# Performance work log

Measured on AMD Instinct MI355X. Metric: run time of the kernel, lower is better.

The kernel has to match this reference:

```python
import jax, jax.numpy as jnp
import numpy as np

ROPE_BASE = 10000.0

def _rope(x):
    # x: (B, T, H, hd); rotate-half RoPE
    B, T, H, hd = x.shape
    half = hd // 2
    inv_freq = 1.0 / (ROPE_BASE ** (jnp.arange(half, dtype=jnp.float32) / half))
    ang = jnp.arange(T, dtype=jnp.float32)[:, None] * inv_freq[None, :]  # (T, half)
    cos = jnp.cos(ang)[None, :, None, :]
    sin = jnp.sin(ang)[None, :, None, :]
    x1, x2 = x[..., :half], x[..., half:]
    return jnp.concatenate([x1 * cos - x2 * sin, x1 * sin + x2 * cos], axis=-1)

def setup_inputs() -> dict:
    key = jax.random.key(0)
    k1, k2, k3 = jax.random.split(key, 3)
    B, T, D = 4, 2048, 2048
    x = jax.random.normal(k1, (B, T, D), dtype=jnp.float32)
    attn_mask = jnp.ones((B, T), dtype=bool)
    w_qkv = jax.random.normal(k2, (3 * D, D), dtype=jnp.float32) * (D ** -0.5)
    w_out = jax.random.normal(k3, (D, D), dtype=jnp.float32) * (D ** -0.5)
    return {"x": x, "attn_mask": attn_mask, "is_causal": 1, "w_qkv": w_qkv, "w_out": w_out}

def reference(x, attn_mask, is_causal, w_qkv, w_out):
    B, T, D = x.shape
    H = 16
    hd = D // H
    qkv = jnp.einsum('btd,ed->bte', x, w_qkv)  # (B, T, 3D)
    q, k, v = jnp.split(qkv, 3, axis=2)
    q = _rope(q.reshape(B, T, H, hd))
    k = _rope(k.reshape(B, T, H, hd))
    v = v.reshape(B, T, H, hd)
    scale = 1.0 / jnp.sqrt(jnp.float32(hd))
    scores = jnp.einsum('bqhd,bkhd->bhqk', q, k) * scale  # (B, H, T, T)
    if is_causal:
        mask = jnp.tril(jnp.ones((T, T), dtype=bool))[None, None]
    else:
        mask = attn_mask[:, None, None, :]  # (B,1,1,T)
    scores = jnp.where(mask, scores, jnp.finfo(scores.dtype).min)
    attn = jax.nn.softmax(scores, axis=-1)
    y = jnp.einsum('bhqk,bkhd->bqhd', attn, v).reshape(B, T, D)
    return jnp.einsum('btd,ed->bte', y, w_out)
```

## Files before the change

kernel.cpp:

```cpp
#include <hip/hip_runtime.h>
#include <stdint.h>
#include <stddef.h>

typedef float f32x4 __attribute__((ext_vector_type(4)));
typedef __bf16 bf16x8 __attribute__((ext_vector_type(8)));
typedef short s16x4 __attribute__((ext_vector_type(4)));

#define DEVI static __device__ __forceinline__

DEVI float bf2f(unsigned short u) {
  unsigned int x = ((unsigned int)u) << 16;
  float f;
  __builtin_memcpy(&f, &x, 4);
  return f;
}
DEVI unsigned short f2bf(float f) {
  unsigned int x;
  __builtin_memcpy(&x, &f, 4);
  unsigned int r = (x + 0x7fffu + ((x >> 16) & 1u)) >> 16;
  return (unsigned short)r;
}

DEVI void async16(const void* g, void* l) {
  __builtin_amdgcn_global_load_lds((__attribute__((address_space(1))) void*)g,
                                   (__attribute__((address_space(3))) void*)l,
                                   16, 0, 0);
}

#define BAR_LGKM()                                          \
  do {                                                      \
    asm volatile("s_waitcnt lgkmcnt(0)" ::: "memory");      \
    __builtin_amdgcn_s_barrier();                           \
    __builtin_amdgcn_sched_barrier(0);                      \
  } while (0)

#define BAR_VM(N)                                               \
  do {                                                          \
    asm volatile("s_waitcnt vmcnt(" #N ")" ::: "memory");       \
    __builtin_amdgcn_s_barrier();                               \
    __builtin_amdgcn_sched_barrier(0);                          \
  } while (0)

__global__ __launch_bounds__(256) void cvt_bf16(const float* __restrict__ in,
                                                unsigned short* __restrict__ out, int n) {
  int i = (blockIdx.x * 256 + threadIdx.x) * 4;
  if (i >= n) return;
  float4 v = *(const float4*)(in + i);
  s16x4 o;
  o[0] = (short)f2bf(v.x);
  o[1] = (short)f2bf(v.y);
  o[2] = (short)f2bf(v.z);
  o[3] = (short)f2bf(v.w);
  *(s16x4*)(out + i) = o;
}

__global__ __launch_bounds__(256) void rope_table(float* __restrict__ tab) {
  int idx = blockIdx.x * 256 + threadIdx.x;
  if (idx >= 2048 * 64) return;
  int tt = idx >> 6, j = idx & 63;
  float inv = powf(10000.0f, -(float)j * (1.0f / 64.0f));
  float ang = (float)tt * inv;
  tab[tt * 128 + j] = cosf(ang);
  tab[tt * 128 + 64 + j] = sinf(ang);
}

__global__ __launch_bounds__(256) void rope_apply(unsigned short* __restrict__ Qg,
                                                  unsigned short* __restrict__ Kg,
                                                  const float* __restrict__ tab) {
  const float S2 = 0.0883883476483184f * 1.44269504088896341f;
  int idx = blockIdx.x * 256 + threadIdx.x;
  int j4 = idx & 15;
  int tt = (idx >> 4) & 2047;
  int bh = idx >> 15;
  size_t base = ((size_t)bh * 2048 + tt) * 128;
  f32x4 c4 = *(const f32x4*)(tab + tt * 128 + j4 * 4);
  f32x4 s4 = *(const f32x4*)(tab + tt * 128 + 64 + j4 * 4);
  s16x4 q1 = *(const s16x4*)(Qg + base + j4 * 4);
  s16x4 q2 = *(const s16x4*)(Qg + base + 64 + j4 * 4);
  s16x4 k1 = *(const s16x4*)(Kg + base + j4 * 4);
  s16x4 k2 = *(const s16x4*)(Kg + base + 64 + j4 * 4);
  s16x4 o1, o2, p1, p2;
#pragma unroll
  for (int r = 0; r < 4; ++r) {
    float c = c4[r], s = s4[r];
    float a = bf2f((unsigned short)q1[r]), b2 = bf2f((unsigned short)q2[r]);
    o1[r] = (short)f2bf((a * c - b2 * s) * S2);
    o2[r] = (short)f2bf((a * s + b2 * c) * S2);
    float ka = bf2f((unsigned short)k1[r]), kb = bf2f((unsigned short)k2[r]);
    p1[r] = (short)f2bf(ka * c - kb * s);
    p2[r] = (short)f2bf(ka * s + kb * c);
  }
  *(s16x4*)(Qg + base + j4 * 4) = o1;
  *(s16x4*)(Qg + base + 64 + j4 * 4) = o2;
  *(s16x4*)(Kg + base + j4 * 4) = p1;
  *(s16x4*)(Kg + base + 64 + j4 * 4) = p2;
}

template <int EPI>
__global__ __launch_bounds__(512) void gemm256(const unsigned short* __restrict__ A,
                                               const unsigned short* __restrict__ B,
                                               float* __restrict__ C, int M, int N, int K,
                                               unsigned short* __restrict__ Q,
                                               unsigned short* __restrict__ Kk,
                                               unsigned short* __restrict__ VT) {
  __shared__ __attribute__((aligned(128))) unsigned short Al[2][2][8192];
  __shared__ __attribute__((aligned(128))) unsigned short Bl[2][2][8192];
  const int t = threadIdx.x;
  const int lane = t & 63;
  const int w = t >> 6, wr = w >> 2, wc = w & 3;
  const int g = lane >> 4, lr = lane & 15;

  const int id = blockIdx.y * gridDim.x + blockIdx.x;
  const int mt = M >> 8, nt = N >> 8;
  const int xcd = id & 7;
  const int local = id >> 3;
  const int rm = mt >> 2, rn = nt >> 1;
  const int bm = ((xcd & 3) * rm + (local % rm)) * 256;
  const int bn = ((xcd >> 2) * rn + (local / rm)) * 256;

  const unsigned short* aptr = A + (size_t)bm * K;
  const unsigned short* bptr = B + (size_t)bn * K;

  const int srow = t >> 3;
  const int sslot = (t & 7) ^ (srow & 7);

#define STG(arr, mat, p, h, kt)                                                   \
  do {                                                                            \
    const unsigned short* _s =                                                    \
        (mat) + (size_t)((h) * 128 + srow) * K + (size_t)(kt) * 64 + sslot * 8;   \
    async16(_s, &arr[p][h][t * 8]);                                               \
    async16(_s + (size_t)64 * K, &arr[p][h][t * 8 + 4096]);                       \
  } while (0)

  const int u0 = ((g ^ (lr & 7)) * 8) + lr * 64;
  const int u1 = (((4 + g) ^ (lr & 7)) * 8) + lr * 64;

#define LDA_(p, mh)                                                               \
  _Pragma("unroll") for (int mf = 0; mf < 4; ++mf) {                              \
    af[mf][0] = *(const bf16x8*)&Al[p][wr][(mh) * 4096 + mf * 1024 + u0];         \
    af[mf][1] = *(const bf16x8*)&Al[p][wr][(mh) * 4096 + mf * 1024 + u1];         \
  }
#define LDB_(dst, p, nh)                                                          \
  _Pragma("unroll") for (int nf = 0; nf < 2; ++nf) {                              \
    dst[nf][0] = *(const bf16x8*)&Bl[p][wc >> 1][(wc & 1) * 4096 + (nh) * 2048 +  \
                                                 nf * 1024 + u0];                 \
    dst[nf][1] = *(const bf16x8*)&Bl[p][wc >> 1][(wc & 1) * 4096 + (nh) * 2048 +  \
                                                 nf * 1024 + u1];                 \
  }
#define MMA_(bsrc, mh, nh)                                                        \
  __builtin_amdgcn_s_setprio(1);                                                  \
  _Pragma("unroll") for (int mf = 0; mf < 4; ++mf)                                \
      _Pragma("unroll") for (int nf = 0; nf < 2; ++nf) {                          \
    acc[(mh) * 4 + mf][(nh) * 2 + nf] = __builtin_amdgcn_mfma_f32_16x16x32_bf16(  \
        af[mf][0], bsrc[nf][0], acc[(mh) * 4 + mf][(nh) * 2 + nf], 0, 0, 0);      \
    acc[(mh) * 4 + mf][(nh) * 2 + nf] = __builtin_amdgcn_mfma_f32_16x16x32_bf16(  \
        af[mf][1], bsrc[nf][1], acc[(mh) * 4 + mf][(nh) * 2 + nf], 0, 0, 0);      \
  }                                                                               \
  __builtin_amdgcn_s_setprio(0);
#define BARR() __builtin_amdgcn_s_barrier();

  f32x4 acc[8][4] = {};
  bf16x8 af[4][2], bfrA[2][2], bfrB[2][2];

  STG(Al, aptr, 0, 0, 0);
  STG(Al, aptr, 0, 1, 0);
  STG(Bl, bptr, 0, 0, 0);
  STG(Bl, bptr, 0, 1, 0);
  STG(Bl, bptr, 1, 0, 1);
  STG(Bl, bptr, 1, 1, 1);
  asm volatile("s_waitcnt vmcnt(4)" ::: "memory");
  __builtin_amdgcn_s_barrier();

  const int NITER = K >> 7;
  for (int i = 0; i < NITER; ++i) {
    const bool G = (i + 1 < NITER);
    const int t1 = 2 * i + 1, t2 = 2 * i + 2, t3 = 2 * i + 3;

    LDA_(0, 0);
    LDB_(bfrA, 0, 0);
    STG(Al, aptr, 1, 0, t1);
    STG(Al, aptr, 1, 1, t1);
    BARR();
    MMA_(bfrA, 0, 0);
    BARR();
    LDB_(bfrB, 0, 1);
    BARR();
    MMA_(bfrB, 0, 1);
    BARR();
    LDA_(0, 1);
    BARR();
    MMA_(bfrB, 1, 1);
    BARR();
    if (G) {
      STG(Bl, bptr, 0, 0, t2);
      asm volatile("s_waitcnt vmcnt(2)" ::: "memory");
    } else {
      asm volatile("s_waitcnt vmcnt(0)" ::: "memory");
    }
    BARR();
    MMA_(bfrA, 1, 0);
    BARR();
    LDA_(1, 0);
    LDB_(bfrA, 1, 0);
    if (G) STG(Bl, bptr, 0, 1, t2);
    BARR();
    MMA_(bfrA, 0, 0);
    BARR();
    LDB_(bfrB, 1, 1);
    if (G) STG(Al, aptr, 0, 0, t2);
    BARR();
    MMA_(bfrB, 0, 1);
    BARR();
    LDA_(1, 1);
    if (G) STG(Al, aptr, 0, 1, t2);
    BARR();
    MMA_(bfrB, 1, 1);
    BARR();
    if (G) {
      STG(Bl, bptr, 1, 0, t3);
      STG(Bl, bptr, 1, 1, t3);
      asm volatile("s_waitcnt vmcnt(4)" ::: "memory");
    }
    BARR();
    MMA_(bfrA, 1, 0);
    BARR();
  }
#undef STG
#undef LDA_
#undef LDB_
#undef MMA_
#undef BARR

  if (EPI == 0) {
#pragma unroll
    for (int mp = 0; mp < 8; ++mp) {
      int m0 = bm + wr * 128 + (mp >> 2) * 64 + (mp & 3) * 16 + g * 4;
#pragma unroll
      for (int nfi = 0; nfi < 4; ++nfi) {
        int n = bn + wc * 64 + (nfi >> 1) * 32 + (nfi & 1) * 16 + lr;
#pragma unroll
        for (int r = 0; r < 4; ++r) C[(size_t)(m0 + r) * N + n] = acc[mp][nfi][r];
      }
    }
  } else {
    const int bi = bm >> 11;
    const int tbase = bm & 2047;
#pragma unroll
    for (int nfi = 0; nfi < 4; ++nfi) {
      int e = bn + wc * 64 + (nfi >> 1) * 32 + (nfi & 1) * 16 + lr;
      int region = e >> 11;
      int e2 = e & 2047;
      int h = e2 >> 7, d = e2 & 127;
      int bh = bi * 16 + h;
#pragma unroll
      for (int mp = 0; mp < 8; ++mp) {
        int trow = tbase + wr * 128 + (mp >> 2) * 64 + (mp & 3) * 16 + g * 4;
        if (region == 2) {
          s16x4 pk;
#pragma unroll
          for (int r = 0; r < 4; ++r) pk[r] = (short)f2bf(acc[mp][nfi][r]);
          *(s16x4*)(VT + ((size_t)bh * 128 + d) * 2048 + trow) = pk;
        } else {
          unsigned short* dst = (region == 0) ? Q : Kk;
#pragma unroll
          for (int r = 0; r < 4; ++r)
            dst[((size_t)bh * 2048 + trow + r) * 128 + d] = f2bf(acc[mp][nfi][r]);
        }
      }
    }
  }
}

__global__ __launch_bounds__(256) void flash_attn(const unsigned short* __restrict__ Qg,
                                                  const unsigned short* __restrict__ Kg,
                                                  const unsigned short* __restrict__ VTg,
                                                  unsigned short* __restrict__ Yg,
                                                  const int* __restrict__ iscausal,
                                                  const unsigned char* __restrict__ amask) {
  __shared__ __attribute__((aligned(128))) unsigned short Ks[2][64 * 128];
  __shared__ __attribute__((aligned(128))) unsigned short Vs[2][128 * 64];
  __shared__ __attribute__((aligned(128))) unsigned short Ps[4][16 * 72];

  const int t = threadIdx.x, lane = t & 63, w = t >> 6;
  const int g = lane >> 4, lr = lane & 15;
  const int id = blockIdx.x;
  const int xcd = id & 7, j5 = id >> 3;
  const int bh = xcd * 8 + (j5 >> 5);
  const int qbi = 31 - (j5 & 31);
  const int b = bh >> 4;
  const int qb = qbi * 64;
  const int causal = iscausal[0] != 0;
  const int nt = causal ? (qbi + 1) : 32;

  const unsigned short* qrow = Qg + ((size_t)bh * 2048 + qb + w * 16 + lr) * 128;
  bf16x8 qf[4];
#pragma unroll
  for (int ds = 0; ds < 4; ++ds) qf[ds] = *(const bf16x8*)(qrow + ds * 32 + g * 8);

  const unsigned short* Kbase = Kg + (size_t)bh * 2048 * 128;
  const unsigned short* Vbase = VTg + (size_t)bh * 128 * 2048;

  const int rK = t >> 4, sK = ((t & 15) ^ rK);
  const int rV = t >> 3, sV = ((t & 7) ^ ((t >> 3) & 7));

#define STAGE(KT, P)                                                                    \
  do {                                                                                  \
    const int _kv = (KT) * 64;                                                          \
    _Pragma("unroll") for (int c = 0; c < 4; ++c)                                       \
        async16(Kbase + (size_t)(_kv + c * 16 + rK) * 128 + sK * 8,                     \
                &Ks[P][c * 2048 + t * 8]);                                              \
    _Pragma("unroll") for (int c = 0; c < 4; ++c)                                       \
        async16(Vbase + (size_t)(c * 32 + rV) * 2048 + _kv + sV * 8,                    \
                &Vs[P][c * 2048 + t * 8]);                                              \
  } while (0)

  unsigned int oi[4] = {0x3F803F80u, 0x3F803F80u, 0x3F803F80u, 0x3F803F80u};
  bf16x8 ones;
  __builtin_memcpy(&ones, oi, 16);

  f32x4 acc[8] = {};
  f32x4 accl = {0.f, 0.f, 0.f, 0.f};
  float mrow[4] = {-1e30f, -1e30f, -1e30f, -1e30f};

  STAGE(0, 0);

  for (int kt = 0; kt < nt; ++kt) {
    const int p = kt & 1;
    const int kv0 = kt * 64;
    if (kt + 1 < nt) {
      STAGE(kt + 1, p ^ 1);
      BAR_VM(8);
    } else {
      BAR_VM(0);
    }

    f32x4 s[4] = {};
    __builtin_amdgcn_s_setprio(1);
#pragma unroll
    for (int cf = 0; cf < 4; ++cf)
#pragma unroll
      for (int ds = 0; ds < 4; ++ds) {
        bf16x8 kf = *(const bf16x8*)(&Ks[p][(cf * 16 + lr) * 128 + (((ds * 4 + g) ^ lr) * 8)]);
        s[cf] = __builtin_amdgcn_mfma_f32_16x16x32_bf16(qf[ds], kf, s[cf], 0, 0, 0);
      }
    __builtin_amdgcn_s_setprio(0);

    const int q0 = qb + w * 16 + g * 4;
    if (causal) {
      if (kt == qbi) {
#pragma unroll
        for (int cf = 0; cf < 4; ++cf) {
          int kvg = kv0 + cf * 16 + lr;
#pragma unroll
          for (int r = 0; r < 4; ++r)
            if (kvg > q0 + r) s[cf][r] = -1e30f;
        }
      }
    } else {
#pragma unroll
      for (int cf = 0; cf < 4; ++cf) {
        int kvg = kv0 + cf * 16 + lr;
        if (!amask[(size_t)b * 2048 + kvg]) {
#pragma unroll
          for (int r = 0; r < 4; ++r) s[cf][r] = -1e30f;
        }
      }
    }

    f32x4 lm;
#pragma unroll
    for (int r = 0; r < 4; ++r)
      lm[r] = fmaxf(fmaxf(s[0][r], s[1][r]), fmaxf(s[2][r], s[3][r]));
    bool ok = true;
#pragma unroll
    for (int r = 0; r < 4; ++r) ok = ok && (lm[r] <= mrow[r] + 8.0f);
    if (!__all(ok)) {
      f32x4 mx = lm;
#pragma unroll
      for (int off = 8; off >= 1; off >>= 1)
#pragma unroll
        for (int r = 0; r < 4; ++r) mx[r] = fmaxf(mx[r], __shfl_xor(mx[r], off));
#pragma unroll
      for (int r = 0; r < 4; ++r) {
        float mn = fmaxf(mrow[r], mx[r]);
        float corr = exp2f(mrow[r] - mn);
        mrow[r] = mn;
        accl[r] *= corr;
#pragma unroll
        for (int jf = 0; jf < 8; ++jf) acc[jf][r] *= corr;
      }
    }

#pragma unroll
    for (int cf = 0; cf < 4; ++cf)
#pragma unroll
      for (int r = 0; r < 4; ++r) s[cf][r] = exp2f(s[cf][r] - mrow[r]);

    unsigned short* Pw = &Ps[w][0];
#pragma unroll
    for (int cf = 0; cf < 4; ++cf)
#pragma unroll
      for (int r = 0; r < 4; ++r) Pw[(g * 4 + r) * 72 + cf * 16 + lr] = f2bf(s[cf][r]);
    asm volatile("s_waitcnt lgkmcnt(0)" ::: "memory");
    __builtin_amdgcn_sched_barrier(0);

    bf16x8 pa0 = *(const bf16x8*)(Pw + lr * 72 + g * 8);
    bf16x8 pa1 = *(const bf16x8*)(Pw + lr * 72 + 32 + g * 8);

    accl = __builtin_amdgcn_mfma_f32_16x16x32_bf16(pa0, ones, accl, 0, 0, 0);
    accl = __builtin_amdgcn_mfma_f32_16x16x32_bf16(pa1, ones, accl, 0, 0, 0);

    __builtin_amdgcn_s_setprio(1);
#pragma unroll
    for (int jf = 0; jf < 8; ++jf) {
      bf16x8 v0 = *(const bf16x8*)(&Vs[p][(jf * 16 + lr) * 64 + ((g ^ (lr & 7)) * 8)]);
      bf16x8 v1 = *(const bf16x8*)(&Vs[p][(jf * 16 + lr) * 64 + (((4 + g) ^ (lr & 7)) * 8)]);
      acc[jf] = __builtin_amdgcn_mfma_f32_16x16x32_bf16(pa0, v0, acc[jf], 0, 0, 0);
      acc[jf] = __builtin_amdgcn_mfma_f32_16x16x32_bf16(pa1, v1, acc[jf], 0, 0, 0);
    }
    __builtin_amdgcn_s_setprio(0);

    BAR_LGKM();
  }
#undef STAGE

  const int h = bh & 15;
  float rl[4];
#pragma unroll
  for (int r = 0; r < 4; ++r) rl[r] = __builtin_amdgcn_rcpf(accl[r]);
#pragma unroll
  for (int jf = 0; jf < 8; ++jf)
#pragma unroll
    for (int r = 0; r < 4; ++r) {
      int tt = qb + w * 16 + g * 4 + r;
      Yg[((size_t)b * 2048 + tt) * 2048 + h * 128 + jf * 16 + lr] = f2bf(acc[jf][r] * rl[r]);
    }
}

extern "C" void kernel_launch(void* const* d_in, const int* in_sizes, int n_in, void* d_out,
                              int out_size, void* d_ws, size_t ws_size, hipStream_t stream) {
  const float* x = (const float*)d_in[0];
  const unsigned char* amask = (const unsigned char*)d_in[1];
  const int* iscausal = (const int*)d_in[2];
  const float* wqkv = (const float*)d_in[3];
  const float* wout = (const float*)d_in[4];
  float* out = (float*)d_out;

  const size_t MT = 8192, D = 2048, ND = 6144;
  unsigned short* xb = (unsigned short*)d_ws;
  unsigned short* wqkvb = xb + MT * D;
  unsigned short* woutb = wqkvb + ND * D;
  unsigned short* q = woutb + D * D;
  unsigned short* k = q + MT * D;
  unsigned short* vt = k + MT * D;
  unsigned short* y = vt + MT * D;
  float* tab = (float*)(y + MT * D);
  if (ws_size < (size_t)(100663296) * 2 + 2048 * 128 * 4) return;

  cvt_bf16<<<dim3(16384), dim3(256), 0, stream>>>(x, xb, (int)(MT * D));
  cvt_bf16<<<dim3(12288), dim3(256), 0, stream>>>(wqkv, wqkvb, (int)(ND * D));
  cvt_bf16<<<dim3(4096), dim3(256), 0, stream>>>(wout, woutb, (int)(D * D));
  rope_table<<<dim3(512), dim3(256), 0, stream>>>(tab);
  gemm256<1><<<dim3(24, 32), dim3(512), 0, stream>>>(xb, wqkvb, nullptr, 8192, 6144, 2048, q, k, vt);
  rope_apply<<<dim3(8192), dim3(256), 0, stream>>>(q, k, tab);
  flash_attn<<<dim3(2048), dim3(256), 0, stream>>>(q, k, vt, y, iscausal, amask);
  gemm256<0><<<dim3(8, 32), dim3(512), 0, stream>>>(y, woutb, out, 8192, 2048, 2048, nullptr,
                                                    nullptr, nullptr);
}
```

Baseline: 486.2 us.

## Enlarge flash-attention query tile to 128 rows with 8 waves and fuse bf16 conversions

Flash attention now runs 512-thread blocks, each covering 128 query rows with 8 waves, so every staged K/V tile is shared by twice as many waves. This halves the K/V global traffic per query. The block-to-tile mapping is reordered to pair long and short causal tiles for load balance, and the causal mask check becomes a per-wave condition. The three fp32-to-bf16 conversion launches are merged into a single kernel to cut launch overhead. In exchange, the larger blocks may lower occupancy and leave wider causal tail imbalance, and the rewritten mask and index logic carries some correctness risk.

```diff
diff --git a/kernel.cpp b/kernel.cpp
--- a/kernel.cpp
+++ b/kernel.cpp
@@ -26,6 +26,13 @@
                                    (__attribute__((address_space(3))) void*)l,
                                    16, 0, 0);
 }
+
+#define BAR_VM(N)                                               \
+  do {                                                          \
+    asm volatile("s_waitcnt vmcnt(" #N ")" ::: "memory");       \
+    __builtin_amdgcn_s_barrier();                               \
+    __builtin_amdgcn_sched_barrier(0);                          \
+  } while (0)
 
 #define BAR_LGKM()                                          \
   do {                                                      \
@@ -34,24 +41,31 @@
     __builtin_amdgcn_sched_barrier(0);                      \
   } while (0)
 
-#define BAR_VM(N)                                               \
-  do {                                                          \
-    asm volatile("s_waitcnt vmcnt(" #N ")" ::: "memory");       \
-    __builtin_amdgcn_s_barrier();                               \
-    __builtin_amdgcn_sched_barrier(0);                          \
-  } while (0)
-
-__global__ __launch_bounds__(256) void cvt_bf16(const float* __restrict__ in,
-                                                unsigned short* __restrict__ out, int n) {
+__global__ __launch_bounds__(256) void cvt3(const float* __restrict__ x,
+                                            const float* __restrict__ wq,
+                                            const float* __restrict__ wo,
+                                            unsigned short* __restrict__ xb,
+                                            unsigned short* __restrict__ wqb,
+                                            unsigned short* __restrict__ wob) {
+  const int n1 = 16777216, n2 = 12582912;
   int i = (blockIdx.x * 256 + threadIdx.x) * 4;
-  if (i >= n) return;
-  float4 v = *(const float4*)(in + i);
+  const float* src;
+  unsigned short* dst;
+  int off;
+  if (i < n1) {
+    src = x; dst = xb; off = i;
+  } else if (i < n1 + n2) {
+    src = wq; dst = wqb; off = i - n1;
+  } else {
+    src = wo; dst = wob; off = i - n1 - n2;
+  }
+  float4 v = *(const float4*)(src + off);
   s16x4 o;
   o[0] = (short)f2bf(v.x);
   o[1] = (short)f2bf(v.y);
   o[2] = (short)f2bf(v.z);
   o[3] = (short)f2bf(v.w);
-  *(s16x4*)(out + i) = o;
+  *(s16x4*)(dst + off) = o;
 }
 
 __global__ __launch_bounds__(256) void rope_table(float* __restrict__ tab) {
@@ -271,7 +285,7 @@
   }
 }
 
-__global__ __launch_bounds__(256) void flash_attn(const unsigned short* __restrict__ Qg,
+__global__ __launch_bounds__(512) void flash_attn(const unsigned short* __restrict__ Qg,
                                                   const unsigned short* __restrict__ Kg,
                                                   const unsigned short* __restrict__ VTg,
                                                   unsigned short* __restrict__ Yg,
@@ -279,18 +293,19 @@
                                                   const unsigned char* __restrict__ amask) {
   __shared__ __attribute__((aligned(128))) unsigned short Ks[2][64 * 128];
   __shared__ __attribute__((aligned(128))) unsigned short Vs[2][128 * 64];
-  __shared__ __attribute__((aligned(128))) unsigned short Ps[4][16 * 72];
+  __shared__ __attribute__((aligned(128))) unsigned short Ps[8][16 * 72];
 
   const int t = threadIdx.x, lane = t & 63, w = t >> 6;
   const int g = lane >> 4, lr = lane & 15;
   const int id = blockIdx.x;
   const int xcd = id & 7, j5 = id >> 3;
-  const int bh = xcd * 8 + (j5 >> 5);
-  const int qbi = 31 - (j5 & 31);
+  const int rr = j5 >> 3;
+  const int qbi = (rr < 4) ? (15 - rr) : (rr < 8) ? (rr - 4) : (rr < 12) ? (19 - rr) : (rr - 8);
+  const int bh = xcd * 8 + (j5 & 7);
   const int b = bh >> 4;
-  const int qb = qbi * 64;
+  const int qb = qbi * 128;
   const int causal = iscausal[0] != 0;
-  const int nt = causal ? (qbi + 1) : 32;
+  const int nt = causal ? (2 * qbi + 2) : 32;
 
   const unsigned short* qrow = Qg + ((size_t)bh * 2048 + qb + w * 16 + lr) * 128;
   bf16x8 qf[4];
@@ -300,18 +315,18 @@
   const unsigned short* Kbase = Kg + (size_t)bh * 2048 * 128;
   const unsigned short* Vbase = VTg + (size_t)bh * 128 * 2048;
 
-  const int rK = t >> 4, sK = ((t & 15) ^ rK);
-  const int rV = t >> 3, sV = ((t & 7) ^ ((t >> 3) & 7));
+  const int rK = t >> 4, sK = (t & 15) ^ (rK & 15);
+  const int rV = t >> 3, sV = (t & 7) ^ (rV & 7);
 
 #define STAGE(KT, P)                                                                    \
   do {                                                                                  \
     const int _kv = (KT) * 64;                                                          \
-    _Pragma("unroll") for (int c = 0; c < 4; ++c)                                       \
-        async16(Kbase + (size_t)(_kv + c * 16 + rK) * 128 + sK * 8,                     \
-                &Ks[P][c * 2048 + t * 8]);                                              \
-    _Pragma("unroll") for (int c = 0; c < 4; ++c)                                       \
-        async16(Vbase + (size_t)(c * 32 + rV) * 2048 + _kv + sV * 8,                    \
-                &Vs[P][c * 2048 + t * 8]);                                              \
+    _Pragma("unroll") for (int c = 0; c < 2; ++c)                                       \
+        async16(Kbase + (size_t)(_kv + c * 32 + rK) * 128 + sK * 8,                     \
+                &Ks[P][c * 4096 + t * 8]);                                              \
+    _Pragma("unroll") for (int c = 0; c < 2; ++c)                                       \
+        async16(Vbase + (size_t)(c * 64 + rV) * 2048 + _kv + sV * 8,                    \
+                &Vs[P][c * 4096 + t * 8]);                                              \
   } while (0)
 
   unsigned int oi[4] = {0x3F803F80u, 0x3F803F80u, 0x3F803F80u, 0x3F803F80u};
@@ -329,7 +344,7 @@
     const int kv0 = kt * 64;
     if (kt + 1 < nt) {
       STAGE(kt + 1, p ^ 1);
-      BAR_VM(8);
+      BAR_VM(4);
     } else {
       BAR_VM(0);
     }
@@ -345,9 +360,10 @@
       }
     __builtin_amdgcn_s_setprio(0);
 
-    const int q0 = qb + w * 16 + g * 4;
+    const int qw = qb + w * 16;
+    const int q0 = qw + g * 4;
     if (causal) {
-      if (kt == qbi) {
+      if (kv0 + 63 > qw) {
 #pragma unroll
         for (int cf = 0; cf < 4; ++cf) {
           int kvg = kv0 + cf * 16 + lr;
@@ -457,13 +473,11 @@
   float* tab = (float*)(y + MT * D);
   if (ws_size < (size_t)(100663296) * 2 + 2048 * 128 * 4) return;
 
-  cvt_bf16<<<dim3(16384), dim3(256), 0, stream>>>(x, xb, (int)(MT * D));
-  cvt_bf16<<<dim3(12288), dim3(256), 0, stream>>>(wqkv, wqkvb, (int)(ND * D));
-  cvt_bf16<<<dim3(4096), dim3(256), 0, stream>>>(wout, woutb, (int)(D * D));
+  cvt3<<<dim3(32768), dim3(256), 0, stream>>>(x, wqkv, wout, xb, wqkvb, woutb);
   rope_table<<<dim3(512), dim3(256), 0, stream>>>(tab);
   gemm256<1><<<dim3(24, 32), dim3(512), 0, stream>>>(xb, wqkvb, nullptr, 8192, 6144, 2048, q, k, vt);
   rope_apply<<<dim3(8192), dim3(256), 0, stream>>>(q, k, tab);
-  flash_attn<<<dim3(2048), dim3(256), 0, stream>>>(q, k, vt, y, iscausal, amask);
+  flash_attn<<<dim3(1024), dim3(512), 0, stream>>>(q, k, vt, y, iscausal, amask);
   gemm256<0><<<dim3(8, 32), dim3(512), 0, stream>>>(y, woutb, out, 8192, 2048, 2048, nullptr,
                                                     nullptr, nullptr);
 }
```

Result: faster. 465.8 us (-4.2%).
